# Optimization experiments

Measured on AMD Instinct MI355X. Metric: run time of the kernel, lower is better.

Reference implementation:

```python
import jax, jax.numpy as jnp
import numpy as np

MODES, WIDTH, DEPTH, IN_F, OUT_F, HID = 8, 16, 3, 1, 1, 64


def setup_inputs() -> dict:
    key = jax.random.key(0)
    ks = jax.random.split(key, 12)
    B, H, W = 8, 512, 512
    scale = 1.0 / (WIDTH * WIDTH)
    inp = {
        'x': jax.random.normal(ks[0], (B, IN_F, H, W), dtype=jnp.float32),
        'fc0_w': jax.random.normal(ks[1], (IN_F, WIDTH), dtype=jnp.float32) * 0.5,
        'fc0_b': jax.random.normal(ks[2], (WIDTH,), dtype=jnp.float32) * 0.1,
        # complex spectral weights stored as real/imag parts, stacked over depth
        'spec_wr': jax.random.normal(ks[3], (DEPTH, WIDTH, WIDTH, MODES, MODES), dtype=jnp.float32) * scale,
        'spec_wi': jax.random.normal(ks[4], (DEPTH, WIDTH, WIDTH, MODES, MODES), dtype=jnp.float32) * scale,
        # 1x1 convs as [depth, out, in] matmuls + bias
        'conv_w': jax.random.normal(ks[5], (DEPTH, WIDTH, WIDTH), dtype=jnp.float32) * 0.25,
        'conv_b': jax.random.normal(ks[6], (DEPTH, WIDTH), dtype=jnp.float32) * 0.1,
        'fc1_w': jax.random.normal(ks[7], (WIDTH, HID), dtype=jnp.float32) * 0.25,
        'fc1_b': jax.random.normal(ks[8], (HID,), dtype=jnp.float32) * 0.1,
        'fc2_w': jax.random.normal(ks[9], (HID, OUT_F), dtype=jnp.float32) * 0.125,
        'fc2_b': jax.random.normal(ks[10], (OUT_F,), dtype=jnp.float32) * 0.1,
    }
    return inp


def _spectral_conv(x, w):
    # x: [B, Ci, H, W] real; w: [Ci, Co, m, m] complex
    B, C, H, W = x.shape
    m = w.shape[2]
    x_ft = jnp.fft.rfft2(x, norm='forward')  # [B, Ci, H, W//2+1]
    out_modes = jnp.einsum('bixy,ioxy->boxy', x_ft[:, :, :m, :m], w)
    out_ft = jnp.zeros((B, w.shape[1], H, W // 2 + 1), dtype=out_modes.dtype)
    out_ft = out_ft.at[:, :, :m, :m].set(out_modes)
    return jnp.fft.irfft2(out_ft, s=(H, W), norm='forward')


def reference(x, fc0_w, fc0_b, spec_wr, spec_wi, conv_w, conv_b, fc1_w, fc1_b, fc2_w, fc2_b):
    # lift: [B,C,H,W] -> channels-last linear -> [B,width,H,W]
    h = jnp.einsum('bchw,cd->bdhw', x, fc0_w) + fc0_b[None, :, None, None]
    for d in range(DEPTH):
        w_c = (spec_wr[d] + 1j * spec_wi[d]).astype(jnp.complex64)
        y = _spectral_conv(h, w_c)
        local = jnp.einsum('bchw,oc->bohw', h, conv_w[d]) + conv_b[d][None, :, None, None]
        h = y + local
    h = jnp.einsum('bchw,cd->bdhw', h, fc1_w) + fc1_b[None, :, None, None]
    h = jax.nn.relu(h)
    out = jnp.einsum('bchw,cd->bdhw', h, fc2_w) + fc2_b[None, :, None, None]
    return out
```

## Files before the change

kernel.cpp:

```cpp
#include <hip/hip_runtime.h>
#include <math.h>

#define NB 8
#define NH 512
#define NW 512
#define ANG512 0.01227184630308513f
#define SPEC_D 16384

#define DEV_SCOPE __HIP_MEMORY_SCOPE_AGENT

__global__ __launch_bounds__(256) void k_pre(const float* __restrict__ x,
                                             float* __restrict__ P,
                                             int* __restrict__ flags) {
    __shared__ float wred[8][16];
    const int tid = threadIdx.x;
    const int w = tid >> 6, lane = tid & 63;
    const int gid = blockIdx.x;
    const int b = gid >> 6, rg = gid & 63;

    if (gid == 0 && tid < 8)
        __hip_atomic_store(&flags[tid * 32], 0, __ATOMIC_RELAXED, DEV_SCOPE);

    #pragma unroll
    for (int rr = 0; rr < 2; ++rr) {
        const int row = rg * 8 + w + 4 * rr;
        const float* xr = x + ((size_t)(b * NH + row)) * NW;

        float p[16];
        #pragma unroll
        for (int j = 0; j < 16; ++j) p[j] = 0.f;

        #pragma unroll
        for (int j = 0; j < 4; ++j) {
            const int ww = lane + (j << 6);
            const float xa = xr[ww], xb = xr[ww + 256];
            const float a = xa + xb, d = xa - xb;
            float c1, s1;
            __sincosf(ANG512 * (float)ww, &s1, &c1);
            p[0] += a;
            p[1] = fmaf(d, c1, p[1]);
            p[9] = fmaf(-d, s1, p[9]);
            const float c2k = 2.f * c1;
            float ckm = 1.f, skm = 0.f, ck = c1, sk = s1;
            #pragma unroll
            for (int k = 2; k < 8; ++k) {
                const float cn = fmaf(c2k, ck, -ckm);
                const float sn = fmaf(c2k, sk, -skm);
                ckm = ck; skm = sk; ck = cn; sk = sn;
                const float v = (k & 1) ? d : a;
                p[k]     = fmaf(v, ck, p[k]);
                p[8 + k] = fmaf(-v, sk, p[8 + k]);
            }
        }
        #pragma unroll
        for (int m = 1; m < 64; m <<= 1) {
            #pragma unroll
            for (int j = 0; j < 16; ++j) p[j] += __shfl_xor(p[j], m);
        }
        if (lane < 16) wred[w + 4 * rr][lane] = p[lane];
    }
    __syncthreads();

    if (tid < 128) {
        const int kx = tid >> 4, q = tid & 15, qm = q & 7;
        float acc = 0.f;
        #pragma unroll
        for (int r = 0; r < 8; ++r) {
            const int row = rg * 8 + r;
            const int m = (kx * row) & 511;
            float cm, s2;
            __sincosf(ANG512 * (float)m, &s2, &cm);
            const float rre = wred[r][qm], rim = wred[r][8 + qm];
            acc += (q < 8) ? (rre * cm + rim * s2)
                           : (rim * cm - rre * s2);
        }
        P[((size_t)((b * 64 + rg) * 8 + kx)) * 16 + q] = acc;
    }
}

__device__ __forceinline__ void phaseC(
        const float* __restrict__ x, const float* __restrict__ AH,
        const float* __restrict__ gvec, const float* __restrict__ Kvec,
        const float* __restrict__ fc2_w, const float* __restrict__ fc2_b,
        float* __restrict__ out, float* sm) {
    float* WHr = sm;
    float* WHi = sm + 2048;

    const int tid = threadIdx.x;
    const int b = blockIdx.x >> 7;
    const int rp = blockIdx.x & 127;
    const int rl = tid >> 6;
    const int row = rp * 4 + rl;
    const int w0 = tid & 63;

    const float* xp = x + ((size_t)(b * NH + row)) * NW + w0;
    float xv[8];
    #pragma unroll
    for (int j = 0; j < 8; ++j) xv[j] = xp[j * 64];

    {
        float c1, s1;
        __sincosf(ANG512 * (float)row, &s1, &c1);
        float ctr[8], str[8];
        ctr[0] = 1.f; str[0] = 0.f; ctr[1] = c1; str[1] = s1;
        const float c2k = 2.f * c1;
        #pragma unroll
        for (int k = 2; k < 8; ++k) {
            ctr[k] = fmaf(c2k, ctr[k - 1], -ctr[k - 2]);
            str[k] = fmaf(c2k, str[k - 1], -str[k - 2]);
        }
        #pragma unroll
        for (int j = 0; j < 8; ++j) {
            const int idx = w0 + j * 64;
            const int hd = idx >> 3, ky = idx & 7;
            const float4* ap = (const float4*)(AH + ((size_t)(b * 64 + hd) * 8 + ky) * 16);
            const float4 a0 = ap[0], a1 = ap[1], a2 = ap[2], a3 = ap[3];
            float wr = a0.x, wi = a0.y;
            wr = fmaf(a0.z, ctr[1], wr); wr = fmaf(-a0.w, str[1], wr);
            wi = fmaf(a0.z, str[1], wi); wi = fmaf(a0.w, ctr[1], wi);
            wr = fmaf(a1.x, ctr[2], wr); wr = fmaf(-a1.y, str[2], wr);
            wi = fmaf(a1.x, str[2], wi); wi = fmaf(a1.y, ctr[2], wi);
            wr = fmaf(a1.z, ctr[3], wr); wr = fmaf(-a1.w, str[3], wr);
            wi = fmaf(a1.z, str[3], wi); wi = fmaf(a1.w, ctr[3], wi);
            wr = fmaf(a2.x, ctr[4], wr); wr = fmaf(-a2.y, str[4], wr);
            wi = fmaf(a2.x, str[4], wi); wi = fmaf(a2.y, ctr[4], wi);
            wr = fmaf(a2.z, ctr[5], wr); wr = fmaf(-a2.w, str[5], wr);
            wi = fmaf(a2.z, str[5], wi); wi = fmaf(a2.w, ctr[5], wi);
            wr = fmaf(a3.x, ctr[6], wr); wr = fmaf(-a3.y, str[6], wr);
            wi = fmaf(a3.x, str[6], wi); wi = fmaf(a3.y, ctr[6], wi);
            wr = fmaf(a3.z, ctr[7], wr); wr = fmaf(-a3.w, str[7], wr);
            wi = fmaf(a3.z, str[7], wi); wi = fmaf(a3.w, ctr[7], wi);
            if (ky == 0) wr += Kvec[hd];
            WHr[rl * 512 + idx] = wr;
            WHi[rl * 512 + idx] = wi;
        }
    }
    __syncthreads();

    {
        float c1, s1;
        __sincosf(ANG512 * (float)w0, &s1, &c1);
        float ct[8], st[8];
        ct[0] = 1.f; st[0] = 0.f; ct[1] = c1; st[1] = s1;
        const float c2k = 2.f * c1;
        #pragma unroll
        for (int k = 2; k < 8; ++k) {
            ct[k] = fmaf(c2k, ct[k - 1], -ct[k - 2]);
            st[k] = fmaf(c2k, st[k - 1], -st[k - 2]);
        }
        const float r2c = 0.70710678118654752f;
        const float* WR = WHr + rl * 512;
        const float* WI = WHi + rl * 512;
        const float fc2b = fc2_b[0];
        float acc[8];
        #pragma unroll
        for (int j = 0; j < 8; ++j) acc[j] = fc2b;

        #pragma unroll 4
        for (int hd = 0; hd < 64; ++hd) {
            const float4* r4 = (const float4*)(WR + hd * 8);
            const float4 wa = r4[0], wb = r4[1];
            const float4* i4 = (const float4*)(WI + hd * 8);
            const float4 va = i4[0], vb = i4[1];
            const float tr0 = wa.x;
            const float tr1 = wa.y * ct[1] - va.y * st[1];
            const float ti1 = wa.y * st[1] + va.y * ct[1];
            const float tr2 = wa.z * ct[2] - va.z * st[2];
            const float ti2 = wa.z * st[2] + va.z * ct[2];
            const float tr3 = wa.w * ct[3] - va.w * st[3];
            const float ti3 = wa.w * st[3] + va.w * ct[3];
            const float tr4 = wb.x * ct[4] - vb.x * st[4];
            const float tr5 = wb.y * ct[5] - vb.y * st[5];
            const float ti5 = wb.y * st[5] + vb.y * ct[5];
            const float tr6 = wb.z * ct[6] - vb.z * st[6];
            const float ti6 = wb.z * st[6] + vb.z * ct[6];
            const float tr7 = wb.w * ct[7] - vb.w * st[7];
            const float ti7 = wb.w * st[7] + vb.w * ct[7];

            const float gh = gvec[hd];
            const float w2 = fc2_w[hd];

            const float A0 = tr0 + tr4, A2 = tr2 + tr6;
            const float E = A0 + A2, D = A0 - A2;
            const float B13 = (tr1 + tr5) + (tr3 + tr7);
            const float U = (ti1 + ti5) - (ti3 + ti7);
            const float s0 = fmaf(gh, xv[0], E + B13);
            const float s2 = fmaf(gh, xv[2], D - U);
            const float s4 = fmaf(gh, xv[4], E - B13);
            const float s6 = fmaf(gh, xv[6], D + U);
            acc[0] = fmaf(fmaxf(s0, 0.f), w2, acc[0]);
            acc[2] = fmaf(fmaxf(s2, 0.f), w2, acc[2]);
            acc[4] = fmaf(fmaxf(s4, 0.f), w2, acc[4]);
            acc[6] = fmaf(fmaxf(s6, 0.f), w2, acc[6]);

            const float P = tr0 - tr4, Q = ti6 - ti2;
            const float E2 = P + Q, D2 = P - Q;
            const float B2 = r2c * (((tr1 - ti1) - (tr5 - ti5)) + ((tr7 + ti7) - (tr3 + ti3)));
            const float U2 = r2c * (((tr1 + ti1) - (tr5 + ti5)) - ((tr3 - ti3) + (ti7 - tr7)));
            const float s1p = fmaf(gh, xv[1], E2 + B2);
            const float s3p = fmaf(gh, xv[3], D2 - U2);
            const float s5p = fmaf(gh, xv[5], E2 - B2);
            const float s7p = fmaf(gh, xv[7], D2 + U2);
            acc[1] = fmaf(fmaxf(s1p, 0.f), w2, acc[1]);
            acc[3] = fmaf(fmaxf(s3p, 0.f), w2, acc[3]);
            acc[5] = fmaf(fmaxf(s5p, 0.f), w2, acc[5]);
            acc[7] = fmaf(fmaxf(s7p, 0.f), w2, acc[7]);
        }
        float* op = out + ((size_t)(b * NH + row)) * NW + w0;
        #pragma unroll
        for (int j = 0; j < 8; ++j) op[j * 64] = acc[j];
    }
}

__global__ __launch_bounds__(256, 4) void k_mh(
        const float* __restrict__ x, const float* __restrict__ P,
        const float* __restrict__ spec_wr, const float* __restrict__ spec_wi,
        const float* __restrict__ conv_w, const float* __restrict__ conv_b,
        const float* __restrict__ fc0_w, const float* __restrict__ fc0_b,
        const float* __restrict__ fc1_w, const float* __restrict__ fc1_b,
        const float* __restrict__ fc2_w, const float* __restrict__ fc2_b,
        float* __restrict__ AH, float* __restrict__ gv, float* __restrict__ Kv,
        int* __restrict__ flags, float* __restrict__ out) {
    __shared__ __align__(16) float sm[4096];
    const int tid = threadIdx.x;
    const int bid = blockIdx.x;

    if (bid < 64) {
        float* red2  = sm;
        float* X2    = sm + 256;
        float* Xr    = sm + 272;
        float* Xi    = sm + 400;
        float* Fr    = sm + 528;
        float* Fi    = sm + 656;
        float* Ar    = sm + 784;
        float* Ai    = sm + 912;
        float* Pm    = sm + 1040;
        float* fc1_s = sm + 1552;
        float* ps    = sm + 2576;

        const int b = bid >> 3;
        const int kx = bid & 7;

        {
            const int o = tid >> 4, c = tid & 15;
            float s = 0.f;
            for (int k = 0; k < 16; ++k)
                s += conv_w[512 + o * 16 + k] * conv_w[256 + k * 16 + c];
            Pm[tid] = s;
        }
        Pm[256 + tid] = conv_w[512 + tid];
        #pragma unroll
        for (int k = 0; k < 4; ++k) fc1_s[tid + k * 256] = fc1_w[tid + k * 256];

        {
            const int q = tid & 15, c = tid >> 4;
            float acc = 0.f;
            #pragma unroll
            for (int m = 0; m < 4; ++m) {
                const int rg = c + 16 * m;
                acc += P[((size_t)((b * 64 + rg) * 8 + kx)) * 16 + q];
            }
            red2[c * 16 + q] = acc;
        }
        __syncthreads();
        if (tid < 16) {
            float s = 0.f;
            #pragma unroll
            for (int c = 0; c < 16; ++c) s += red2[c * 16 + tid];
            X2[tid] = s;
        }
        __syncthreads();

        const bool act = (tid < 128);
        const int o = tid >> 3, ky = tid & 7;
        if (act) {
            const float inv = 1.f / (512.f * 512.f);
            float xr0 = fc0_w[o] * X2[ky] * inv;
            float xi0 = fc0_w[o] * X2[8 + ky] * inv;
            if (kx == 0 && ky == 0) xr0 += fc0_b[o];
            Xr[o * 8 + ky] = xr0; Xi[o * 8 + ky] = xi0;
            Ar[o * 8 + ky] = 0.f; Ai[o * 8 + ky] = 0.f;
        }
        __syncthreads();

        for (int dd = 0; dd < 3; ++dd) {
            if (act) {
                float fr = 0.f, fi = 0.f;
                const float* wrp = spec_wr + (size_t)dd * SPEC_D + o * 64 + kx * 8 + ky;
                const float* wip = spec_wi + (size_t)dd * SPEC_D + o * 64 + kx * 8 + ky;
                #pragma unroll
                for (int i = 0; i < 16; ++i) {
                    const float wre = wrp[i * 1024];
                    const float wim = wip[i * 1024];
                    const float xr0 = Xr[i * 8 + ky], xi0 = Xi[i * 8 + ky];
                    fr += xr0 * wre - xi0 * wim;
                    fi += xr0 * wim + xi0 * wre;
                }
                Fr[o * 8 + ky] = fr; Fi[o * 8 + ky] = fi;
            }
            __syncthreads();
            float xnr = 0.f, xni = 0.f;
            if (act) {
                float ar, ai;
                if (dd == 2) {
                    ar = Fr[o * 8 + ky]; ai = Fi[o * 8 + ky];
                } else {
                    ar = 0.f; ai = 0.f;
                    #pragma unroll
                    for (int c = 0; c < 16; ++c) {
                        const float pv = Pm[dd * 256 + o * 16 + c];
                        ar = fmaf(pv, Fr[c * 8 + ky], ar);
                        ai = fmaf(pv, Fi[c * 8 + ky], ai);
                    }
                }
                Ar[o * 8 + ky] += ar; Ai[o * 8 + ky] += ai;
                if (dd < 2) {
                    const float fr0 = Fr[o * 8 + ky], fi0 = Fi[o * 8 + ky];
                    if (ky == 0) {
                        if (kx == 0) { xnr = fr0; xni = 0.f; }
                        else         { xnr = 0.5f * fr0; xni = 0.5f * fi0; }
                    } else { xnr = fr0; xni = fi0; }
                    #pragma unroll
                    for (int c = 0; c < 16; ++c) {
                        const float cc = conv_w[dd * 256 + o * 16 + c];
                        xnr = fmaf(cc, Xr[c * 8 + ky], xnr);
                        xni = fmaf(cc, Xi[c * 8 + ky], xni);
                    }
                    if (kx == 0 && ky == 0) xnr += conv_b[dd * 16 + o];
                }
            }
            __syncthreads();
            if (act && dd < 2) { Xr[o * 8 + ky] = xnr; Xi[o * 8 + ky] = xni; }
            __syncthreads();
        }

        #pragma unroll
        for (int k2 = 0; k2 < 2; ++k2) {
            const int idx = tid + k2 * 256;
            const int hd = idx >> 3, ky2 = idx & 7;
            float ar = 0.f, ai = 0.f;
            #pragma unroll
            for (int c = 0; c < 16; ++c) {
                const float f = fc1_s[c * 64 + hd];
                ar = fmaf(f, Ar[c * 8 + ky2], ar);
                ai = fmaf(f, Ai[c * 8 + ky2], ai);
            }
            const float ck = (ky2 == 0) ? 1.f : 2.f;
            const size_t off = ((((size_t)(b * 64 + hd)) * 8 + ky2) * 8 + kx) * 2;
            __hip_atomic_store(&AH[off],     ck * ar, __ATOMIC_RELAXED, DEV_SCOPE);
            __hip_atomic_store(&AH[off + 1], ck * ai, __ATOMIC_RELAXED, DEV_SCOPE);
        }

        if (kx == 0) {
            if (tid < 16) {
                float su = 0.f, sb = 0.f;
                for (int c = 0; c < 16; ++c) {
                    su += conv_w[tid * 16 + c] * fc0_w[c];
                    sb += conv_w[tid * 16 + c] * fc0_b[c];
                }
                ps[tid] = su; ps[16 + tid] = sb;
            }
            __syncthreads();
            if (tid < 16) {
                float dv = 0.f, ev = conv_b[32 + tid];
                for (int k = 0; k < 16; ++k) {
                    dv += Pm[tid * 16 + k] * ps[k];
                    ev += Pm[tid * 16 + k] * (ps[16 + k] + conv_b[k]);
                    ev += conv_w[512 + tid * 16 + k] * conv_b[16 + k];
                }
                ps[32 + tid] = dv; ps[48 + tid] = ev;
            }
            __syncthreads();
            if (tid < 64) {
                float g = 0.f, K = fc1_b[tid];
                for (int c = 0; c < 16; ++c) {
                    g = fmaf(fc1_w[c * 64 + tid], ps[32 + c], g);
                    K = fmaf(fc1_w[c * 64 + tid], ps[48 + c], K);
                }
                __hip_atomic_store(&gv[b * 64 + tid], g, __ATOMIC_RELAXED, DEV_SCOPE);
                __hip_atomic_store(&Kv[b * 64 + tid], K, __ATOMIC_RELAXED, DEV_SCOPE);
            }
        }
        __syncthreads();
        if (tid == 0)
            __hip_atomic_fetch_add(&flags[b * 32], 1, __ATOMIC_RELEASE, DEV_SCOPE);
    }

    const int cb = bid >> 7;
    if (tid == 0) {
        while (__hip_atomic_load(&flags[cb * 32], __ATOMIC_RELAXED, DEV_SCOPE) < 8)
            __builtin_amdgcn_s_sleep(8);
    }
    __syncthreads();

    phaseC(x, AH, gv + cb * 64, Kv + cb * 64, fc2_w, fc2_b, out, sm);
}

extern "C" void kernel_launch(void* const* d_in, const int* in_sizes, int n_in,
                              void* d_out, int out_size, void* d_ws, size_t ws_size,
                              hipStream_t stream) {
    const float* x       = (const float*)d_in[0];
    const float* fc0_w   = (const float*)d_in[1];
    const float* fc0_b   = (const float*)d_in[2];
    const float* spec_wr = (const float*)d_in[3];
    const float* spec_wi = (const float*)d_in[4];
    const float* conv_w  = (const float*)d_in[5];
    const float* conv_b  = (const float*)d_in[6];
    const float* fc1_w   = (const float*)d_in[7];
    const float* fc1_b   = (const float*)d_in[8];
    const float* fc2_w   = (const float*)d_in[9];
    const float* fc2_b   = (const float*)d_in[10];
    float* outp = (float*)d_out;

    char* ws = (char*)d_ws;
    float* P   = (float*)ws;
    float* AH  = (float*)(ws + 262144);
    float* gv  = (float*)(ws + 524288);
    float* Kv  = (float*)(ws + 526336);
    int*  flg  = (int*)(ws + 528384);

    k_pre<<<512, 256, 0, stream>>>(x, P, flg);
    k_mh<<<1024, 256, 0, stream>>>(x, P, spec_wr, spec_wi, conv_w, conv_b,
                                   fc0_w, fc0_b, fc1_w, fc1_b, fc2_w, fc2_b,
                                   AH, gv, Kv, flg, outp);
}
```

Before: 143.8 us.

## Split fused kernel into three launches and run head inverse-DFT on bf16 MFMA

Replaces the single persistent kernel, which used flag spin-waits between the mode-mixing blocks and the head blocks, with separate k_modes and k_head launches that rely on stream ordering. The per-pixel inverse DFT over 8 column modes plus the fc1/relu/fc2 head is recast as 16x16x32 bf16 MFMA products. Precision is kept by splitting both the twiddle table and the row coefficients into hi/lo bf16 pairs. This moves the dominant FMA work onto matrix units, at the cost of an extra launch, bf16 split error and more LDS setup per block.

```diff
diff --git a/kernel.cpp b/kernel.cpp
--- a/kernel.cpp
+++ b/kernel.cpp
@@ -7,19 +7,24 @@
 #define ANG512 0.01227184630308513f
 #define SPEC_D 16384
 
-#define DEV_SCOPE __HIP_MEMORY_SCOPE_AGENT
+typedef __attribute__((ext_vector_type(8))) short  bf16x8;
+typedef __attribute__((ext_vector_type(4))) float  f32x4;
+
+__device__ __forceinline__ unsigned short f2bf(float f) {
+    unsigned u = __float_as_uint(f);
+    return (unsigned short)((u + 0x7FFFu + ((u >> 16) & 1u)) >> 16);
+}
+__device__ __forceinline__ float bf2f(unsigned short h) {
+    return __uint_as_float(((unsigned)h) << 16);
+}
 
 __global__ __launch_bounds__(256) void k_pre(const float* __restrict__ x,
-                                             float* __restrict__ P,
-                                             int* __restrict__ flags) {
+                                             float* __restrict__ P) {
     __shared__ float wred[8][16];
     const int tid = threadIdx.x;
     const int w = tid >> 6, lane = tid & 63;
     const int gid = blockIdx.x;
     const int b = gid >> 6, rg = gid & 63;
-
-    if (gid == 0 && tid < 8)
-        __hip_atomic_store(&flags[tid * 32], 0, __ATOMIC_RELAXED, DEV_SCOPE);
 
     #pragma unroll
     for (int rr = 0; rr < 2; ++rr) {
@@ -78,25 +83,219 @@
     }
 }
 
-__device__ __forceinline__ void phaseC(
+__global__ __launch_bounds__(256) void k_modes(
+        const float* __restrict__ P,
+        const float* __restrict__ spec_wr, const float* __restrict__ spec_wi,
+        const float* __restrict__ conv_w, const float* __restrict__ conv_b,
+        const float* __restrict__ fc0_w, const float* __restrict__ fc0_b,
+        const float* __restrict__ fc1_w, const float* __restrict__ fc1_b,
+        float* __restrict__ AH, float* __restrict__ gv, float* __restrict__ Kv) {
+    __shared__ __align__(16) float sm[2640];
+    float* red2  = sm;
+    float* X2    = sm + 256;
+    float* Xr    = sm + 272;
+    float* Xi    = sm + 400;
+    float* Fr    = sm + 528;
+    float* Fi    = sm + 656;
+    float* Ar    = sm + 784;
+    float* Ai    = sm + 912;
+    float* Pm    = sm + 1040;
+    float* fc1_s = sm + 1552;
+    float* ps    = sm + 2576;
+
+    const int tid = threadIdx.x;
+    const int bid = blockIdx.x;
+    const int b = bid >> 3;
+    const int kx = bid & 7;
+
+    {
+        const int o = tid >> 4, c = tid & 15;
+        float s = 0.f;
+        for (int k = 0; k < 16; ++k)
+            s += conv_w[512 + o * 16 + k] * conv_w[256 + k * 16 + c];
+        Pm[tid] = s;
+    }
+    Pm[256 + tid] = conv_w[512 + tid];
+    #pragma unroll
+    for (int k = 0; k < 4; ++k) fc1_s[tid + k * 256] = fc1_w[tid + k * 256];
+
+    {
+        const int q = tid & 15, c = tid >> 4;
+        float acc = 0.f;
+        #pragma unroll
+        for (int m = 0; m < 4; ++m) {
+            const int rg = c + 16 * m;
+            acc += P[((size_t)((b * 64 + rg) * 8 + kx)) * 16 + q];
+        }
+        red2[c * 16 + q] = acc;
+    }
+    __syncthreads();
+    if (tid < 16) {
+        float s = 0.f;
+        #pragma unroll
+        for (int c = 0; c < 16; ++c) s += red2[c * 16 + tid];
+        X2[tid] = s;
+    }
+    __syncthreads();
+
+    const bool act = (tid < 128);
+    const int o = tid >> 3, ky = tid & 7;
+    if (act) {
+        const float inv = 1.f / (512.f * 512.f);
+        float xr0 = fc0_w[o] * X2[ky] * inv;
+        float xi0 = fc0_w[o] * X2[8 + ky] * inv;
+        if (kx == 0 && ky == 0) xr0 += fc0_b[o];
+        Xr[o * 8 + ky] = xr0; Xi[o * 8 + ky] = xi0;
+        Ar[o * 8 + ky] = 0.f; Ai[o * 8 + ky] = 0.f;
+    }
+    __syncthreads();
+
+    for (int dd = 0; dd < 3; ++dd) {
+        if (act) {
+            float fr = 0.f, fi = 0.f;
+            const float* wrp = spec_wr + (size_t)dd * SPEC_D + o * 64 + kx * 8 + ky;
+            const float* wip = spec_wi + (size_t)dd * SPEC_D + o * 64 + kx * 8 + ky;
+            #pragma unroll
+            for (int i = 0; i < 16; ++i) {
+                const float wre = wrp[i * 1024];
+                const float wim = wip[i * 1024];
+                const float xr0 = Xr[i * 8 + ky], xi0 = Xi[i * 8 + ky];
+                fr += xr0 * wre - xi0 * wim;
+                fi += xr0 * wim + xi0 * wre;
+            }
+            Fr[o * 8 + ky] = fr; Fi[o * 8 + ky] = fi;
+        }
+        __syncthreads();
+        float xnr = 0.f, xni = 0.f;
+        if (act) {
+            float ar, ai;
+            if (dd == 2) {
+                ar = Fr[o * 8 + ky]; ai = Fi[o * 8 + ky];
+            } else {
+                ar = 0.f; ai = 0.f;
+                #pragma unroll
+                for (int c = 0; c < 16; ++c) {
+                    const float pv = Pm[dd * 256 + o * 16 + c];
+                    ar = fmaf(pv, Fr[c * 8 + ky], ar);
+                    ai = fmaf(pv, Fi[c * 8 + ky], ai);
+                }
+            }
+            Ar[o * 8 + ky] += ar; Ai[o * 8 + ky] += ai;
+            if (dd < 2) {
+                const float fr0 = Fr[o * 8 + ky], fi0 = Fi[o * 8 + ky];
+                if (ky == 0) {
+                    if (kx == 0) { xnr = fr0; xni = 0.f; }
+                    else         { xnr = 0.5f * fr0; xni = 0.5f * fi0; }
+                } else { xnr = fr0; xni = fi0; }
+                #pragma unroll
+                for (int c = 0; c < 16; ++c) {
+                    const float cc = conv_w[dd * 256 + o * 16 + c];
+                    xnr = fmaf(cc, Xr[c * 8 + ky], xnr);
+                    xni = fmaf(cc, Xi[c * 8 + ky], xni);
+                }
+                if (kx == 0 && ky == 0) xnr += conv_b[dd * 16 + o];
+            }
+        }
+        __syncthreads();
+        if (act && dd < 2) { Xr[o * 8 + ky] = xnr; Xi[o * 8 + ky] = xni; }
+        __syncthreads();
+    }
+
+    #pragma unroll
+    for (int k2 = 0; k2 < 2; ++k2) {
+        const int idx = tid + k2 * 256;
+        const int hd = idx >> 3, ky2 = idx & 7;
+        float ar = 0.f, ai = 0.f;
+        #pragma unroll
+        for (int c = 0; c < 16; ++c) {
+            const float f = fc1_s[c * 64 + hd];
+            ar = fmaf(f, Ar[c * 8 + ky2], ar);
+            ai = fmaf(f, Ai[c * 8 + ky2], ai);
+        }
+        const float ck = (ky2 == 0) ? 1.f : 2.f;
+        const size_t off = ((((size_t)(b * 64 + hd)) * 8 + ky2) * 8 + kx) * 2;
+        AH[off]     = ck * ar;
+        AH[off + 1] = ck * ai;
+    }
+
+    if (kx == 0) {
+        if (tid < 16) {
+            float su = 0.f, sb = 0.f;
+            for (int c = 0; c < 16; ++c) {
+                su += conv_w[tid * 16 + c] * fc0_w[c];
+                sb += conv_w[tid * 16 + c] * fc0_b[c];
+            }
+            ps[tid] = su; ps[16 + tid] = sb;
+        }
+        __syncthreads();
+        if (tid < 16) {
+            float dv = 0.f, ev = conv_b[32 + tid];
+            for (int k = 0; k < 16; ++k) {
+                dv += Pm[tid * 16 + k] * ps[k];
+                ev += Pm[tid * 16 + k] * (ps[16 + k] + conv_b[k]);
+                ev += conv_w[512 + tid * 16 + k] * conv_b[16 + k];
+            }
+            ps[32 + tid] = dv; ps[48 + tid] = ev;
+        }
+        __syncthreads();
+        if (tid < 64) {
+            float g = 0.f, K = fc1_b[tid];
+            for (int c = 0; c < 16; ++c) {
+                g = fmaf(fc1_w[c * 64 + tid], ps[32 + c], g);
+                K = fmaf(fc1_w[c * 64 + tid], ps[48 + c], K);
+            }
+            gv[b * 64 + tid] = g;
+            Kv[b * 64 + tid] = K;
+        }
+    }
+}
+
+__global__ __launch_bounds__(256, 3) void k_head(
         const float* __restrict__ x, const float* __restrict__ AH,
-        const float* __restrict__ gvec, const float* __restrict__ Kvec,
+        const float* __restrict__ gv, const float* __restrict__ Kv,
         const float* __restrict__ fc2_w, const float* __restrict__ fc2_b,
-        float* __restrict__ out, float* sm) {
-    float* WHr = sm;
-    float* WHi = sm + 2048;
-
-    const int tid = threadIdx.x;
-    const int b = blockIdx.x >> 7;
-    const int rp = blockIdx.x & 127;
-    const int rl = tid >> 6;
-    const int row = rp * 4 + rl;
-    const int w0 = tid & 63;
-
-    const float* xp = x + ((size_t)(b * NH + row)) * NW + w0;
-    float xv[8];
+        float* __restrict__ out) {
+    __shared__ __align__(16) unsigned short Ehi[2][512][8];
+    __shared__ __align__(16) unsigned short Elo[2][512][8];
+    __shared__ __align__(16) unsigned short Apk[4][4][64][8];
+
+    const int tid  = threadIdx.x;
+    const int lane = tid & 63;
+    const int rl   = tid >> 6;
+    const int b    = blockIdx.x >> 7;
+    const int rp   = blockIdx.x & 127;
+    const int row  = rp * 4 + rl;
+
     #pragma unroll
-    for (int j = 0; j < 8; ++j) xv[j] = xp[j * 64];
+    for (int pxi = 0; pxi < 2; ++pxi) {
+        const int px = tid + pxi * 256;
+        float c1, s1;
+        __sincosf(ANG512 * (float)px, &s1, &c1);
+        float ck = 1.f, sk = 0.f;
+        #pragma unroll
+        for (int k = 0; k < 8; ++k) {
+            const float e0 = ck, e1 = -sk;
+            const unsigned short h0 = f2bf(e0), h1 = f2bf(e1);
+            Ehi[0][px][k] = h0;  Elo[0][px][k] = f2bf(e0 - bf2f(h0));
+            Ehi[1][px][k] = h1;  Elo[1][px][k] = f2bf(e1 - bf2f(h1));
+            const float cn = ck * c1 - sk * s1;
+            const float sn = sk * c1 + ck * s1;
+            ck = cn; sk = sn;
+        }
+    }
+
+    float ghr[16], w2r[16];
+    {
+        const int lg = lane >> 4;
+        #pragma unroll
+        for (int t = 0; t < 4; ++t)
+            #pragma unroll
+            for (int v = 0; v < 4; ++v) {
+                const int hd = t * 16 + lg * 4 + v;
+                ghr[t * 4 + v] = gv[b * 64 + hd];
+                w2r[t * 4 + v] = fc2_w[hd];
+            }
+    }
 
     {
         float c1, s1;
@@ -111,7 +310,7 @@
         }
         #pragma unroll
         for (int j = 0; j < 8; ++j) {
-            const int idx = w0 + j * 64;
+            const int idx = lane + j * 64;
             const int hd = idx >> 3, ky = idx & 7;
             const float4* ap = (const float4*)(AH + ((size_t)(b * 64 + hd) * 8 + ky) * 16);
             const float4 a0 = ap[0], a1 = ap[1], a2 = ap[2], a3 = ap[3];
@@ -130,270 +329,58 @@
             wi = fmaf(a3.x, str[6], wi); wi = fmaf(a3.y, ctr[6], wi);
             wr = fmaf(a3.z, ctr[7], wr); wr = fmaf(-a3.w, str[7], wr);
             wi = fmaf(a3.z, str[7], wi); wi = fmaf(a3.w, ctr[7], wi);
-            if (ky == 0) wr += Kvec[hd];
-            WHr[rl * 512 + idx] = wr;
-            WHi[rl * 512 + idx] = wi;
+            if (ky == 0) wr += Kv[b * 64 + hd];
+            const unsigned short hr = f2bf(wr), hi_ = f2bf(wi);
+            Apk[rl][0][hd][ky] = hr;
+            Apk[rl][1][hd][ky] = hi_;
+            Apk[rl][2][hd][ky] = f2bf(wr - bf2f(hr));
+            Apk[rl][3][hd][ky] = f2bf(wi - bf2f(hi_));
         }
     }
     __syncthreads();
 
+    bf16x8 a1[4], a2[4];
     {
-        float c1, s1;
-        __sincosf(ANG512 * (float)w0, &s1, &c1);
-        float ct[8], st[8];
-        ct[0] = 1.f; st[0] = 0.f; ct[1] = c1; st[1] = s1;
-        const float c2k = 2.f * c1;
-        #pragma unroll
-        for (int k = 2; k < 8; ++k) {
-            ct[k] = fmaf(c2k, ct[k - 1], -ct[k - 2]);
-            st[k] = fmaf(c2k, st[k - 1], -st[k - 2]);
-        }
-        const float r2c = 0.70710678118654752f;
-        const float* WR = WHr + rl * 512;
-        const float* WI = WHi + rl * 512;
-        const float fc2b = fc2_b[0];
-        float acc[8];
-        #pragma unroll
-        for (int j = 0; j < 8; ++j) acc[j] = fc2b;
-
-        #pragma unroll 4
-        for (int hd = 0; hd < 64; ++hd) {
-            const float4* r4 = (const float4*)(WR + hd * 8);
-            const float4 wa = r4[0], wb = r4[1];
-            const float4* i4 = (const float4*)(WI + hd * 8);
-            const float4 va = i4[0], vb = i4[1];
-            const float tr0 = wa.x;
-            const float tr1 = wa.y * ct[1] - va.y * st[1];
-            const float ti1 = wa.y * st[1] + va.y * ct[1];
-            const float tr2 = wa.z * ct[2] - va.z * st[2];
-            const float ti2 = wa.z * st[2] + va.z * ct[2];
-            const float tr3 = wa.w * ct[3] - va.w * st[3];
-            const float ti3 = wa.w * st[3] + va.w * ct[3];
-            const float tr4 = wb.x * ct[4] - vb.x * st[4];
-            const float tr5 = wb.y * ct[5] - vb.y * st[5];
-            const float ti5 = wb.y * st[5] + vb.y * ct[5];
-            const float tr6 = wb.z * ct[6] - vb.z * st[6];
-            const float ti6 = wb.z * st[6] + vb.z * ct[6];
-            const float tr7 = wb.w * ct[7] - vb.w * st[7];
-            const float ti7 = wb.w * st[7] + vb.w * ct[7];
-
-            const float gh = gvec[hd];
-            const float w2 = fc2_w[hd];
-
-            const float A0 = tr0 + tr4, A2 = tr2 + tr6;
-            const float E = A0 + A2, D = A0 - A2;
-            const float B13 = (tr1 + tr5) + (tr3 + tr7);
-            const float U = (ti1 + ti5) - (ti3 + ti7);
-            const float s0 = fmaf(gh, xv[0], E + B13);
-            const float s2 = fmaf(gh, xv[2], D - U);
-            const float s4 = fmaf(gh, xv[4], E - B13);
-            const float s6 = fmaf(gh, xv[6], D + U);
-            acc[0] = fmaf(fmaxf(s0, 0.f), w2, acc[0]);
-            acc[2] = fmaf(fmaxf(s2, 0.f), w2, acc[2]);
-            acc[4] = fmaf(fmaxf(s4, 0.f), w2, acc[4]);
-            acc[6] = fmaf(fmaxf(s6, 0.f), w2, acc[6]);
-
-            const float P = tr0 - tr4, Q = ti6 - ti2;
-            const float E2 = P + Q, D2 = P - Q;
-            const float B2 = r2c * (((tr1 - ti1) - (tr5 - ti5)) + ((tr7 + ti7) - (tr3 + ti3)));
-            const float U2 = r2c * (((tr1 + ti1) - (tr5 + ti5)) - ((tr3 - ti3) + (ti7 - tr7)));
-            const float s1p = fmaf(gh, xv[1], E2 + B2);
-            const float s3p = fmaf(gh, xv[3], D2 - U2);
-            const float s5p = fmaf(gh, xv[5], E2 - B2);
-            const float s7p = fmaf(gh, xv[7], D2 + U2);
-            acc[1] = fmaf(fmaxf(s1p, 0.f), w2, acc[1]);
-            acc[3] = fmaf(fmaxf(s3p, 0.f), w2, acc[3]);
-            acc[5] = fmaf(fmaxf(s5p, 0.f), w2, acc[5]);
-            acc[7] = fmaf(fmaxf(s7p, 0.f), w2, acc[7]);
-        }
-        float* op = out + ((size_t)(b * NH + row)) * NW + w0;
-        #pragma unroll
-        for (int j = 0; j < 8; ++j) op[j * 64] = acc[j];
-    }
-}
-
-__global__ __launch_bounds__(256, 4) void k_mh(
-        const float* __restrict__ x, const float* __restrict__ P,
-        const float* __restrict__ spec_wr, const float* __restrict__ spec_wi,
-        const float* __restrict__ conv_w, const float* __restrict__ conv_b,
-        const float* __restrict__ fc0_w, const float* __restrict__ fc0_b,
-        const float* __restrict__ fc1_w, const float* __restrict__ fc1_b,
-        const float* __restrict__ fc2_w, const float* __restrict__ fc2_b,
-        float* __restrict__ AH, float* __restrict__ gv, float* __restrict__ Kv,
-        int* __restrict__ flags, float* __restrict__ out) {
-    __shared__ __align__(16) float sm[4096];
-    const int tid = threadIdx.x;
-    const int bid = blockIdx.x;
-
-    if (bid < 64) {
-        float* red2  = sm;
-        float* X2    = sm + 256;
-        float* Xr    = sm + 272;
-        float* Xi    = sm + 400;
-        float* Fr    = sm + 528;
-        float* Fi    = sm + 656;
-        float* Ar    = sm + 784;
-        float* Ai    = sm + 912;
-        float* Pm    = sm + 1040;
-        float* fc1_s = sm + 1552;
-        float* ps    = sm + 2576;
-
-        const int b = bid >> 3;
-        const int kx = bid & 7;
-
-        {
-            const int o = tid >> 4, c = tid & 15;
-            float s = 0.f;
-            for (int k = 0; k < 16; ++k)
-                s += conv_w[512 + o * 16 + k] * conv_w[256 + k * 16 + c];
-            Pm[tid] = s;
-        }
-        Pm[256 + tid] = conv_w[512 + tid];
-        #pragma unroll
-        for (int k = 0; k < 4; ++k) fc1_s[tid + k * 256] = fc1_w[tid + k * 256];
-
-        {
-            const int q = tid & 15, c = tid >> 4;
-            float acc = 0.f;
+        const int kb = lane >> 4, m = lane & 15;
+        const bf16x8 zz = {0, 0, 0, 0, 0, 0, 0, 0};
+        #pragma unroll
+        for (int t = 0; t < 4; ++t) {
+            a1[t] = *(const bf16x8*)&Apk[rl][kb][t * 16 + m][0];
+            a2[t] = (lane < 32) ? a1[t] : zz;
+        }
+    }
+
+    const int eb = (lane >> 4) & 1, n = lane & 15;
+    const float fc2b = fc2_b[0];
+    const float* xrow = x + ((size_t)(b * NH + row)) * NW;
+    float* orow = out + ((size_t)(b * NH + row)) * NW;
+
+    #pragma unroll 2
+    for (int pxt = 0; pxt < 32; ++pxt) {
+        const int px = pxt * 16 + n;
+        const bf16x8 b1 = *(const bf16x8*)&Ehi[eb][px][0];
+        const bf16x8 b2 = *(const bf16x8*)&Elo[eb][px][0];
+        f32x4 c[4];
+        #pragma unroll
+        for (int t = 0; t < 4; ++t) {
+            c[t] = (f32x4){0.f, 0.f, 0.f, 0.f};
+            c[t] = __builtin_amdgcn_mfma_f32_16x16x32_bf16(a1[t], b1, c[t], 0, 0, 0);
+            c[t] = __builtin_amdgcn_mfma_f32_16x16x32_bf16(a2[t], b2, c[t], 0, 0, 0);
+        }
+        const float xpx = xrow[px];
+        float val = 0.f;
+        #pragma unroll
+        for (int t = 0; t < 4; ++t)
             #pragma unroll
-            for (int m = 0; m < 4; ++m) {
-                const int rg = c + 16 * m;
-                acc += P[((size_t)((b * 64 + rg) * 8 + kx)) * 16 + q];
-            }
-            red2[c * 16 + q] = acc;
-        }
-        __syncthreads();
-        if (tid < 16) {
-            float s = 0.f;
-            #pragma unroll
-            for (int c = 0; c < 16; ++c) s += red2[c * 16 + tid];
-            X2[tid] = s;
-        }
-        __syncthreads();
-
-        const bool act = (tid < 128);
-        const int o = tid >> 3, ky = tid & 7;
-        if (act) {
-            const float inv = 1.f / (512.f * 512.f);
-            float xr0 = fc0_w[o] * X2[ky] * inv;
-            float xi0 = fc0_w[o] * X2[8 + ky] * inv;
-            if (kx == 0 && ky == 0) xr0 += fc0_b[o];
-            Xr[o * 8 + ky] = xr0; Xi[o * 8 + ky] = xi0;
-            Ar[o * 8 + ky] = 0.f; Ai[o * 8 + ky] = 0.f;
-        }
-        __syncthreads();
-
-        for (int dd = 0; dd < 3; ++dd) {
-            if (act) {
-                float fr = 0.f, fi = 0.f;
-                const float* wrp = spec_wr + (size_t)dd * SPEC_D + o * 64 + kx * 8 + ky;
-                const float* wip = spec_wi + (size_t)dd * SPEC_D + o * 64 + kx * 8 + ky;
-                #pragma unroll
-                for (int i = 0; i < 16; ++i) {
-                    const float wre = wrp[i * 1024];
-                    const float wim = wip[i * 1024];
-                    const float xr0 = Xr[i * 8 + ky], xi0 = Xi[i * 8 + ky];
-                    fr += xr0 * wre - xi0 * wim;
-                    fi += xr0 * wim + xi0 * wre;
-                }
-                Fr[o * 8 + ky] = fr; Fi[o * 8 + ky] = fi;
-            }
-            __syncthreads();
-            float xnr = 0.f, xni = 0.f;
-            if (act) {
-                float ar, ai;
-                if (dd == 2) {
-                    ar = Fr[o * 8 + ky]; ai = Fi[o * 8 + ky];
-                } else {
-                    ar = 0.f; ai = 0.f;
-                    #pragma unroll
-                    for (int c = 0; c < 16; ++c) {
-                        const float pv = Pm[dd * 256 + o * 16 + c];
-                        ar = fmaf(pv, Fr[c * 8 + ky], ar);
-                        ai = fmaf(pv, Fi[c * 8 + ky], ai);
-                    }
-                }
-                Ar[o * 8 + ky] += ar; Ai[o * 8 + ky] += ai;
-                if (dd < 2) {
-                    const float fr0 = Fr[o * 8 + ky], fi0 = Fi[o * 8 + ky];
-                    if (ky == 0) {
-                        if (kx == 0) { xnr = fr0; xni = 0.f; }
-                        else         { xnr = 0.5f * fr0; xni = 0.5f * fi0; }
-                    } else { xnr = fr0; xni = fi0; }
-                    #pragma unroll
-                    for (int c = 0; c < 16; ++c) {
-                        const float cc = conv_w[dd * 256 + o * 16 + c];
-                        xnr = fmaf(cc, Xr[c * 8 + ky], xnr);
-                        xni = fmaf(cc, Xi[c * 8 + ky], xni);
-                    }
-                    if (kx == 0 && ky == 0) xnr += conv_b[dd * 16 + o];
-                }
-            }
-            __syncthreads();
-            if (act && dd < 2) { Xr[o * 8 + ky] = xnr; Xi[o * 8 + ky] = xni; }
-            __syncthreads();
-        }
-
-        #pragma unroll
-        for (int k2 = 0; k2 < 2; ++k2) {
-            const int idx = tid + k2 * 256;
-            const int hd = idx >> 3, ky2 = idx & 7;
-            float ar = 0.f, ai = 0.f;
-            #pragma unroll
-            for (int c = 0; c < 16; ++c) {
-                const float f = fc1_s[c * 64 + hd];
-                ar = fmaf(f, Ar[c * 8 + ky2], ar);
-                ai = fmaf(f, Ai[c * 8 + ky2], ai);
-            }
-            const float ck = (ky2 == 0) ? 1.f : 2.f;
-            const size_t off = ((((size_t)(b * 64 + hd)) * 8 + ky2) * 8 + kx) * 2;
-            __hip_atomic_store(&AH[off],     ck * ar, __ATOMIC_RELAXED, DEV_SCOPE);
-            __hip_atomic_store(&AH[off + 1], ck * ai, __ATOMIC_RELAXED, DEV_SCOPE);
-        }
-
-        if (kx == 0) {
-            if (tid < 16) {
-                float su = 0.f, sb = 0.f;
-                for (int c = 0; c < 16; ++c) {
-                    su += conv_w[tid * 16 + c] * fc0_w[c];
-                    sb += conv_w[tid * 16 + c] * fc0_b[c];
-                }
-                ps[tid] = su; ps[16 + tid] = sb;
-            }
-            __syncthreads();
-            if (tid < 16) {
-                float dv = 0.f, ev = conv_b[32 + tid];
-                for (int k = 0; k < 16; ++k) {
-                    dv += Pm[tid * 16 + k] * ps[k];
-                    ev += Pm[tid * 16 + k] * (ps[16 + k] + conv_b[k]);
-                    ev += conv_w[512 + tid * 16 + k] * conv_b[16 + k];
-                }
-                ps[32 + tid] = dv; ps[48 + tid] = ev;
-            }
-            __syncthreads();
-            if (tid < 64) {
-                float g = 0.f, K = fc1_b[tid];
-                for (int c = 0; c < 16; ++c) {
-                    g = fmaf(fc1_w[c * 64 + tid], ps[32 + c], g);
-                    K = fmaf(fc1_w[c * 64 + tid], ps[48 + c], K);
-                }
-                __hip_atomic_store(&gv[b * 64 + tid], g, __ATOMIC_RELAXED, DEV_SCOPE);
-                __hip_atomic_store(&Kv[b * 64 + tid], K, __ATOMIC_RELAXED, DEV_SCOPE);
-            }
-        }
-        __syncthreads();
-        if (tid == 0)
-            __hip_atomic_fetch_add(&flags[b * 32], 1, __ATOMIC_RELEASE, DEV_SCOPE);
-    }
-
-    const int cb = bid >> 7;
-    if (tid == 0) {
-        while (__hip_atomic_load(&flags[cb * 32], __ATOMIC_RELAXED, DEV_SCOPE) < 8)
-            __builtin_amdgcn_s_sleep(8);
-    }
-    __syncthreads();
-
-    phaseC(x, AH, gv + cb * 64, Kv + cb * 64, fc2_w, fc2_b, out, sm);
+            for (int v = 0; v < 4; ++v) {
+                float s = fmaf(ghr[t * 4 + v], xpx, c[t][v]);
+                s = fmaxf(s, 0.f);
+                val = fmaf(s, w2r[t * 4 + v], val);
+            }
+        val += __shfl_xor(val, 16);
+        val += __shfl_xor(val, 32);
+        if (lane < 16) orow[pxt * 16 + lane] = val + fc2b;
+    }
 }
 
 extern "C" void kernel_launch(void* const* d_in, const int* in_sizes, int n_in,
@@ -413,14 +400,13 @@
     float* outp = (float*)d_out;
 
     char* ws = (char*)d_ws;
-    float* P   = (float*)ws;
-    float* AH  = (float*)(ws + 262144);
-    float* gv  = (float*)(ws + 524288);
-    float* Kv  = (float*)(ws + 526336);
-    int*  flg  = (int*)(ws + 528384);
-
-    k_pre<<<512, 256, 0, stream>>>(x, P, flg);
-    k_mh<<<1024, 256, 0, stream>>>(x, P, spec_wr, spec_wi, conv_w, conv_b,
-                                   fc0_w, fc0_b, fc1_w, fc1_b, fc2_w, fc2_b,
-                                   AH, gv, Kv, flg, outp);
-}
+    float* P  = (float*)ws;
+    float* AH = (float*)(ws + 262144);
+    float* gv = (float*)(ws + 524288);
+    float* Kv = (float*)(ws + 526336);
+
+    k_pre<<<512, 256, 0, stream>>>(x, P);
+    k_modes<<<64, 256, 0, stream>>>(P, spec_wr, spec_wi, conv_w, conv_b,
+                                    fc0_w, fc0_b, fc1_w, fc1_b, AH, gv, Kv);
+    k_head<<<1024, 256, 0, stream>>>(x, AH, gv, Kv, fc2_w, fc2_b, outp);
+}
```

New measurement: 133.7 us. -7.1%, faster.
